# Kernel optimization log

Hardware: AMD Instinct MI355X
Metric: run time of the kernel (lower is better)

The kernel has to match this reference:

```python
import jax, jax.numpy as jnp
import numpy as np

D_MODEL = 256
K = 50                      # angle_k neighbors
TEMPERATURE = 10000.0
SCALE = 1.0
NUM_POS_FEATS = D_MODEL // 3 // 2 * 2   # 84
PADDING = D_MODEL - NUM_POS_FEATS * 3   # 4


def setup_inputs() -> dict:
    key = jax.random.key(0)
    ks = jax.random.split(key, 6)
    B, N, M = 4, 20000, 1024
    points = jax.random.normal(ks[0], (B, N, 3), jnp.float32)
    nodes = jax.random.normal(ks[1], (B, M, 3), jnp.float32)
    pn = jax.random.normal(ks[2], (B, N, 3), jnp.float32)
    nn_ = jax.random.normal(ks[3], (B, M, 3), jnp.float32)
    pn = pn / jnp.linalg.norm(pn, axis=-1, keepdims=True)
    nn_ = nn_ / jnp.linalg.norm(nn_, axis=-1, keepdims=True)
    W = jax.random.normal(ks[4], (4, D_MODEL), jnp.float32) * 0.5  # glo_proj weight (in,out)
    b = jax.random.normal(ks[5], (D_MODEL,), jnp.float32) * 0.1    # glo_proj bias
    return {"points": points, "nodes": nodes, "points_normals": pn,
            "nodes_normals": nn_, "W": W, "b": b}


def _signed_angle(v1, v2):
    sin_v = jnp.linalg.norm(jnp.cross(v1, v2), axis=-1)
    cos_v = jnp.sum(v1 * v2, axis=-1)
    ang = jnp.arctan2(sin_v, cos_v)
    return jnp.where(cos_v < 0, -ang, ang)


def _ppf_features(points, nodes, pn, nn_):
    # points (N,3), nodes (M,3); KNN gather then PPF angles -> (M,K,4)
    d2 = jnp.sum((nodes[:, None, :] - points[None, :, :]) ** 2, axis=-1)  # (M,N)
    _, knn_idx = jax.lax.top_k(-d2, K)          # (M,K) nearest points per node
    knn_pts = points[knn_idx]                   # (M,K,3) irregular gather
    knn_nrm = pn[knn_idx]                       # (M,K,3)
    ij = knn_pts - nodes[:, None, :]            # (M,K,3)
    d = jnp.linalg.norm(ij, axis=-1) * SCALE    # (M,K)
    n1 = jnp.broadcast_to(nn_[:, None, :], ij.shape)
    a_n1_d = _signed_angle(ij, n1)
    a_n2_d = _signed_angle(-ij, knn_nrm)
    a_n1_n2 = _signed_angle(n1, knn_nrm)
    return jnp.stack([d, a_n1_d, a_n2_d, a_n1_n2], axis=-1)  # (M,K,4)


def reference(points, nodes, points_normals, nodes_normals, W, b):
    # --- global embedding: PPF features -> Linear(4,D) -> max over K ---
    feats = jax.vmap(_ppf_features)(points, nodes, points_normals, nodes_normals)
    feats = jax.lax.stop_gradient(feats)        # original uses @torch.no_grad()
    glob = jnp.max(feats @ W + b, axis=-2)      # (B,M,D)
    # --- local embedding: sinusoidal position encoding of node coords ---
    dim_t = jnp.arange(NUM_POS_FEATS, dtype=jnp.float32)
    dim_t = TEMPERATURE ** (2.0 * jnp.floor(dim_t / 2.0) / NUM_POS_FEATS)
    pos = (nodes * SCALE)[..., None] / dim_t    # (B,M,3,F)
    pos_emb = jnp.stack([jnp.sin(pos[..., 0::2]), jnp.cos(pos[..., 1::2])], axis=-1)
    pos_emb = pos_emb.reshape(nodes.shape[0], nodes.shape[1], -1)  # (B,M,3*F)
    pos_emb = jnp.pad(pos_emb, [(0, 0), (0, 0), (0, PADDING)])     # (B,M,D)
    return glob, pos_emb
```

## Files before the change

kernel.cpp:

```cpp
#include <hip/hip_runtime.h>

#define N_PTS    20000
#define M_NODES  1024
#define BATCH    4
#define NNODE    (BATCH * M_NODES)
#define K_NN     50
#define D_MODEL  256
#define NPF      84
#define CAP      768
#define SELWIN   96
#define NSMP     2048
#define WLO      26
#define WHI      50
#define TN        32
#define KB_PPT    10
#define KB_CHUNK  2560
#define KB_NCHUNK 8
#define LOCAL_CAP 128
#define OVF_FLAG  (1 << 20)

__device__ __forceinline__ float signed_angle(float ax, float ay, float az,
                                              float bx, float by, float bz) {
    float cx = ay * bz - az * by;
    float cy = az * bx - ax * bz;
    float cz = ax * by - ay * bx;
    float s = sqrtf(cx * cx + cy * cy + cz * cz);
    float c = ax * bx + ay * by + az * bz;
    float a = atan2f(s, c);
    return (c < 0.0f) ? -a : a;
}

__global__ __launch_bounds__(256) void ka_thresh(
    const float* __restrict__ points, const float* __restrict__ nodes,
    float* __restrict__ tws, int* __restrict__ gcount, float* __restrict__ out)
{
    __shared__ float s3[NSMP * 3];
    const int tid  = threadIdx.x;
    const int w    = tid >> 6;
    const int lane = tid & 63;
    const int bm   = blockIdx.x * 4 + w;
    const int b    = bm >> 10;
    const float* pts = points + (size_t)b * N_PTS * 3;

    {
        const float4* src = (const float4*)pts;
        float4* dst = (float4*)s3;
        #pragma unroll
        for (int k = 0; k < 6; ++k)
            dst[tid + 256 * k] = src[tid + 256 * k];
    }
    __syncthreads();

    const float nx = nodes[(size_t)bm * 3 + 0];
    const float ny = nodes[(size_t)bm * 3 + 1];
    const float nz = nodes[(size_t)bm * 3 + 2];

    unsigned short keys[32];
    #pragma unroll
    for (int s = 0; s < 32; ++s) {
        int j = lane + 64 * s;
        float dx = s3[3 * j + 0] - nx;
        float dy = s3[3 * j + 1] - ny;
        float dz = s3[3 * j + 2] - nz;
        float d2 = dx * dx + dy * dy + dz * dz;
        keys[s] = (unsigned short)(__float_as_uint(d2) >> 16);
    }

    unsigned lo = 0, hi = 0x7F81u, v = 0;
    for (int it = 0; it < 16; ++it) {
        unsigned mid = lo + ((hi - lo) >> 1);
        int c = 0;
        #pragma unroll
        for (int s = 0; s < 32; ++s) c += (int)((unsigned)keys[s] < mid);
        for (int off = 32; off; off >>= 1) c += __shfl_down(c, off);
        c = __shfl(c, 0);
        if (c >= WLO && c <= WHI) { v = mid; break; }
        if (c < WLO) lo = mid; else hi = mid;
        if (hi - lo <= 1u) break;
    }
    if (v == 0) v = hi;
    if (lane == 0) { tws[bm] = __uint_as_float(v << 16); gcount[bm] = 0; }

    #pragma unroll
    for (int r = 0; r < 4; ++r) {
        int d = lane + 64 * r;
        float pv = 0.0f;
        if (d < 3 * NPF) {
            int c2 = d / NPF, rr = d - c2 * NPF, i = rr >> 1;
            float nc = (c2 == 0) ? nx : ((c2 == 1) ? ny : nz);
            const float L2_10000 = 13.287712379549449f;
            float tinv = exp2f(-L2_10000 * (float)i / 42.0f);
            float x = nc * tinv;
            pv = (rr & 1) ? cosf(x) : sinf(x);
        }
        out[(size_t)NNODE * D_MODEL + (size_t)bm * D_MODEL + d] = pv;
    }
}

__global__ __launch_bounds__(256) void kb_scan(
    const float* __restrict__ points, const float* __restrict__ nodes,
    const float* __restrict__ tws, int* __restrict__ gcount,
    unsigned short* __restrict__ cand)
{
    __shared__ float4 snd[TN];
    __shared__ unsigned short sbuf[TN][LOCAL_CAP];
    __shared__ int scnt[TN];
    __shared__ int sbase[TN];

    const int tile = blockIdx.x;
    const int ch   = blockIdx.y;
    const int ngb  = tile * TN;
    const int b    = ngb >> 10;
    const int tid  = threadIdx.x;
    const float* pts = points + (size_t)b * N_PTS * 3;

    if (tid < TN) {
        int ng = ngb + tid;
        snd[tid] = make_float4(nodes[(size_t)ng * 3 + 0], nodes[(size_t)ng * 3 + 1],
                               nodes[(size_t)ng * 3 + 2], tws[ng]);
        scnt[tid] = 0;
    }
    __syncthreads();

    const int base0 = ch * KB_CHUNK;
    float px[KB_PPT], py[KB_PPT], pz[KB_PPT];
    #pragma unroll
    for (int p = 0; p < KB_PPT; ++p) {
        int j = base0 + p * 256 + tid;
        bool ok = j < N_PTS;
        int jj = ok ? j : 0;
        float vx = pts[jj * 3 + 0], vy = pts[jj * 3 + 1], vz = pts[jj * 3 + 2];
        px[p] = ok ? vx : 1e18f;
        py[p] = ok ? vy : 1e18f;
        pz[p] = ok ? vz : 1e18f;
    }

    for (int n = 0; n < TN; ++n) {
        float4 nd = snd[n];
        unsigned m = 0;
        #pragma unroll
        for (int p = 0; p < KB_PPT; ++p) {
            float dx = px[p] - nd.x, dy = py[p] - nd.y, dz = pz[p] - nd.z;
            float d2 = dx * dx + dy * dy + dz * dz;
            m |= (d2 < nd.w) ? (1u << p) : 0u;
        }
        if (m) {
            do {
                int p = __ffs(m) - 1; m &= m - 1;
                int q = atomicAdd(&scnt[n], 1);
                if (q < LOCAL_CAP)
                    sbuf[n][q] = (unsigned short)(base0 + p * 256 + tid);
            } while (m);
        }
    }
    __syncthreads();

    if (tid < TN) {
        int c = scnt[tid];
        int flag = (c > LOCAL_CAP) ? OVF_FLAG : 0;
        sbase[tid] = atomicAdd(&gcount[ngb + tid], c + flag);
        scnt[tid] = (c < LOCAL_CAP) ? c : LOCAL_CAP;
    }
    __syncthreads();

    const int wv = tid >> 6, lane = tid & 63;
    #pragma unroll
    for (int nn = 0; nn < TN / 4; ++nn) {
        int n = wv * (TN / 4) + nn;
        int c = scnt[n], gb = sbase[n];
        for (int s = lane; s < c; s += 64) {
            int pos = gb + s;
            if (pos < CAP)
                cand[(size_t)(ngb + n) * CAP + pos] = sbuf[n][s];
        }
    }
}

__global__ __launch_bounds__(256) void kc_select(
    const float* __restrict__ points, const float* __restrict__ nodes,
    const float* __restrict__ pnrm, const float* __restrict__ nnrm,
    const float* __restrict__ W, const float* __restrict__ bias,
    const float* __restrict__ tws, const int* __restrict__ gcount,
    const unsigned short* __restrict__ cand, float* __restrict__ out)
{
    __shared__ unsigned long long skeys[4][CAP];
    __shared__ float4 f4v[4][K_NN];
    __shared__ unsigned short selidx[4][K_NN];

    const int tid  = threadIdx.x;
    const int wv   = tid >> 6;
    const int lane = tid & 63;
    const int bm   = blockIdx.x * 4 + wv;
    const int b    = bm >> 10;
    const float* pts = points + (size_t)b * N_PTS * 3;
    const float* pnr = pnrm   + (size_t)b * N_PTS * 3;
    const float nx  = nodes[(size_t)bm * 3 + 0];
    const float ny  = nodes[(size_t)bm * 3 + 1];
    const float nz  = nodes[(size_t)bm * 3 + 2];
    const float n1x = nnrm[(size_t)bm * 3 + 0];
    const float n1y = nnrm[(size_t)bm * 3 + 1];
    const float n1z = nnrm[(size_t)bm * 3 + 2];

    auto d2bits = [&](int i) -> unsigned int {
        float dx = pts[i * 3 + 0] - nx;
        float dy = pts[i * 3 + 1] - ny;
        float dz = pts[i * 3 + 2] - nz;
        return __float_as_uint(dx * dx + dy * dy + dz * dz);
    };

    if (lane < K_NN) selidx[wv][lane] = 0;

    const unsigned long long INVALID = ~0ull;
    int cnt = gcount[bm];
    int nsel = 0;

    if (cnt >= K_NN && cnt <= CAP) {
        const unsigned short* cp = cand + (size_t)bm * CAP;
        unsigned long long key[12];
        #pragma unroll
        for (int r = 0; r < 12; ++r) {
            int s = r * 64 + lane;
            key[r] = INVALID;
            if (s < cnt) {
                int i = (int)cp[s];
                key[r] = ((unsigned long long)d2bits(i) << 32) | (unsigned int)i;
            }
        }

        unsigned long long tcut = INVALID;
        bool conv = (cnt <= SELWIN);
        if (!conv) {
            unsigned lo = 0, hi = __float_as_uint(tws[bm]);
            for (int it = 0; it < 32 && !conv; ++it) {
                unsigned mid = lo + ((hi - lo) >> 1);
                unsigned long long tm = (unsigned long long)mid << 32;
                int c = 0;
                #pragma unroll
                for (int r = 0; r < 12; ++r)
                    c += (int)__popcll(__ballot(key[r] < tm));
                if (c >= K_NN && c <= SELWIN) { tcut = tm; conv = true; }
                else if (c < K_NN) lo = mid;
                else hi = mid;
                if (hi - lo <= 1u) break;
            }
        }

        int run = 0;
        #pragma unroll
        for (int r = 0; r < 12; ++r) {
            bool p = key[r] < tcut;
            unsigned long long mask = __ballot(p);
            if (p) {
                int q = run + (int)__popcll(mask & ((1ull << lane) - 1ull));
                skeys[wv][q] = key[r];
            }
            run += (int)__popcll(mask);
        }
        nsel = run;
    } else {
        unsigned tb = __float_as_uint(tws[bm]);
        unsigned lo = 0, hi = 0x7F000000u, good = 0;
        bool haveLo = false, haveHi = false;
        if (cnt < K_NN) { lo = tb; haveLo = true; }
        else            { hi = tb; haveHi = true; }
        unsigned cur = tb;
        for (int a = 0; a < 40 && !good; ++a) {
            if (haveLo && !haveHi) {
                cur = (cur < 0x7E800000u) ? cur + 0x00800000u : 0x7F000000u;
            } else if (haveHi && !haveLo) {
                cur = (cur >= 0x00800000u) ? cur - 0x00800000u : (cur >> 1);
            } else {
                cur = lo + ((hi - lo) >> 1);
                if (hi - lo <= 1u) { good = hi; break; }
            }
            float tf = __uint_as_float(cur);
            int c = 0;
            for (int i0 = lane; i0 < N_PTS; i0 += 64) {
                float dx = pts[i0 * 3 + 0] - nx;
                float dy = pts[i0 * 3 + 1] - ny;
                float dz = pts[i0 * 3 + 2] - nz;
                c += (int)(dx * dx + dy * dy + dz * dz < tf);
            }
            for (int off = 32; off; off >>= 1) c += __shfl_down(c, off);
            c = __shfl(c, 0);
            if (c >= K_NN && c <= CAP) good = cur;
            else if (c < K_NN) { lo = cur; haveLo = true; }
            else               { hi = cur; haveHi = true; }
        }
        if (!good) good = haveHi ? hi : 0x7F000000u;
        int run = 0;
        for (int base = 0; base < N_PTS; base += 64) {
            int i0 = base + lane;
            bool pred = false;
            unsigned kb2 = 0;
            if (i0 < N_PTS) { kb2 = d2bits(i0); pred = kb2 < good; }
            unsigned long long mask = __ballot(pred);
            if (pred) {
                int q = run + (int)__popcll(mask & ((1ull << lane) - 1ull));
                if (q < CAP)
                    skeys[wv][q] = ((unsigned long long)kb2 << 32) | (unsigned int)i0;
            }
            run += (int)__popcll(mask);
        }
        nsel = run < CAP ? run : CAP;
    }
    __syncthreads();

    for (int s = lane; s < nsel; s += 64) {
        unsigned long long mk = skeys[wv][s];
        int rank = 0;
        for (int j = 0; j < nsel; ++j) rank += (int)(skeys[wv][j] < mk);
        if (rank < K_NN) selidx[wv][rank] = (unsigned short)mk;
    }
    __syncthreads();

    if (lane < K_NN) {
        int i = (int)selidx[wv][lane];
        float pxx = pts[i * 3 + 0], pyy = pts[i * 3 + 1], pzz = pts[i * 3 + 2];
        float qx = pnr[i * 3 + 0], qy = pnr[i * 3 + 1], qz = pnr[i * 3 + 2];
        float ijx = pxx - nx, ijy = pyy - ny, ijz = pzz - nz;
        float d = sqrtf(ijx * ijx + ijy * ijy + ijz * ijz);
        f4v[wv][lane] = make_float4(d,
                                    signed_angle(ijx, ijy, ijz, n1x, n1y, n1z),
                                    signed_angle(-ijx, -ijy, -ijz, qx, qy, qz),
                                    signed_angle(n1x, n1y, n1z, qx, qy, qz));
    }
    __syncthreads();

    {
        float w0[4], w1[4], w2[4], w3[4], bb[4], mx[4];
        #pragma unroll
        for (int q = 0; q < 4; ++q) {
            int d = lane + 64 * q;
            w0[q] = W[d]; w1[q] = W[D_MODEL + d];
            w2[q] = W[2 * D_MODEL + d]; w3[q] = W[3 * D_MODEL + d];
            bb[q] = bias[d]; mx[q] = -INFINITY;
        }
        #pragma unroll 5
        for (int k = 0; k < K_NN; ++k) {
            float4 f = f4v[wv][k];
            #pragma unroll
            for (int q = 0; q < 4; ++q)
                mx[q] = fmaxf(mx[q], f.x * w0[q] + f.y * w1[q] + f.z * w2[q] + f.w * w3[q]);
        }
        #pragma unroll
        for (int q = 0; q < 4; ++q)
            out[(size_t)bm * D_MODEL + lane + 64 * q] = mx[q] + bb[q];
    }
}

extern "C" void kernel_launch(void* const* d_in, const int* in_sizes, int n_in,
                              void* d_out, int out_size, void* d_ws, size_t ws_size,
                              hipStream_t stream) {
    const float* points = (const float*)d_in[0];
    const float* nodes  = (const float*)d_in[1];
    const float* pn     = (const float*)d_in[2];
    const float* nn     = (const float*)d_in[3];
    const float* W      = (const float*)d_in[4];
    const float* bias   = (const float*)d_in[5];
    float* out = (float*)d_out;

    char* ws = (char*)d_ws;
    float* tws = (float*)ws;
    int* gcount = (int*)(ws + 16384);
    unsigned short* cand = (unsigned short*)(ws + 32768);

    ka_thresh<<<dim3(NNODE / 4), dim3(256), 0, stream>>>(points, nodes, tws, gcount, out);
    kb_scan<<<dim3(NNODE / TN, KB_NCHUNK), dim3(256), 0, stream>>>(points, nodes, tws, gcount, cand);
    kc_select<<<dim3(NNODE / 4), dim3(256), 0, stream>>>(points, nodes, pn, nn, W, bias,
                                                         tws, gcount, cand, out);
}
```

Baseline: 74.20 us.

## Restructure KNN candidate scan with expanded-distance FMAs and contiguous vector loads

The candidate scan kernel now gives each thread 8 contiguous points, loaded as six float4 reads, instead of strided scalar loads. Point distance tests use the expanded form |p|^2 - 2p·n < t - |n|^2, evaluated with FMAs. Nodes are processed four at a time, held in registers rather than read from shared memory. The threshold is relaxed slightly so rounding in the expanded form cannot drop true neighbours, at the cost of a few extra candidates. The chunk geometry changes to 10 chunks of 2048 points to match the new per-thread layout.

```diff
diff --git a/kernel.cpp b/kernel.cpp
--- a/kernel.cpp
+++ b/kernel.cpp
@@ -13,9 +13,9 @@
 #define WLO      26
 #define WHI      50
 #define TN        32
-#define KB_PPT    10
-#define KB_CHUNK  2560
-#define KB_NCHUNK 8
+#define KB_PPT    8
+#define KB_CHUNK  2048
+#define KB_NCHUNK 10
 #define LOCAL_CAP 128
 #define OVF_FLAG  (1 << 20)
 
@@ -102,7 +102,6 @@
     const float* __restrict__ tws, int* __restrict__ gcount,
     unsigned short* __restrict__ cand)
 {
-    __shared__ float4 snd[TN];
     __shared__ unsigned short sbuf[TN][LOCAL_CAP];
     __shared__ int scnt[TN];
     __shared__ int sbase[TN];
@@ -114,43 +113,62 @@
     const int tid  = threadIdx.x;
     const float* pts = points + (size_t)b * N_PTS * 3;
 
-    if (tid < TN) {
-        int ng = ngb + tid;
-        snd[tid] = make_float4(nodes[(size_t)ng * 3 + 0], nodes[(size_t)ng * 3 + 1],
-                               nodes[(size_t)ng * 3 + 2], tws[ng]);
-        scnt[tid] = 0;
-    }
-    __syncthreads();
-
-    const int base0 = ch * KB_CHUNK;
-    float px[KB_PPT], py[KB_PPT], pz[KB_PPT];
+    if (tid < TN) scnt[tid] = 0;
+    __syncthreads();
+
+    const int j0 = ch * KB_CHUNK + tid * KB_PPT;
+    float px[KB_PPT], py[KB_PPT], pz[KB_PPT], pp[KB_PPT];
+    if (j0 < N_PTS) {
+        const float4* s4 = (const float4*)(pts + (size_t)j0 * 3);
+        float4 v0 = s4[0], v1 = s4[1], v2 = s4[2], v3 = s4[3], v4 = s4[4], v5 = s4[5];
+        px[0]=v0.x; py[0]=v0.y; pz[0]=v0.z;
+        px[1]=v0.w; py[1]=v1.x; pz[1]=v1.y;
+        px[2]=v1.z; py[2]=v1.w; pz[2]=v2.x;
+        px[3]=v2.y; py[3]=v2.z; pz[3]=v2.w;
+        px[4]=v3.x; py[4]=v3.y; pz[4]=v3.z;
+        px[5]=v3.w; py[5]=v4.x; pz[5]=v4.y;
+        px[6]=v4.z; py[6]=v4.w; pz[6]=v5.x;
+        px[7]=v5.y; py[7]=v5.z; pz[7]=v5.w;
+    } else {
+        #pragma unroll
+        for (int p = 0; p < KB_PPT; ++p) { px[p]=1e18f; py[p]=1e18f; pz[p]=1e18f; }
+    }
     #pragma unroll
-    for (int p = 0; p < KB_PPT; ++p) {
-        int j = base0 + p * 256 + tid;
-        bool ok = j < N_PTS;
-        int jj = ok ? j : 0;
-        float vx = pts[jj * 3 + 0], vy = pts[jj * 3 + 1], vz = pts[jj * 3 + 2];
-        px[p] = ok ? vx : 1e18f;
-        py[p] = ok ? vy : 1e18f;
-        pz[p] = ok ? vz : 1e18f;
-    }
-
-    for (int n = 0; n < TN; ++n) {
-        float4 nd = snd[n];
-        unsigned m = 0;
+    for (int p = 0; p < KB_PPT; ++p)
+        pp[p] = px[p]*px[p] + py[p]*py[p] + pz[p]*pz[p];
+
+    for (int n0 = 0; n0 < TN; n0 += 4) {
+        float ax[4], ay[4], az[4], rhs[4];
+        #pragma unroll
+        for (int g = 0; g < 4; ++g) {
+            int ng = ngb + n0 + g;
+            float nx = nodes[ng * 3 + 0];
+            float ny = nodes[ng * 3 + 1];
+            float nz = nodes[ng * 3 + 2];
+            float t  = tws[ng];
+            ax[g] = -2.0f * nx; ay[g] = -2.0f * ny; az[g] = -2.0f * nz;
+            rhs[g] = t * 1.0001f + 3e-5f - (nx*nx + ny*ny + nz*nz);
+        }
+        unsigned msk[4] = {0u, 0u, 0u, 0u};
         #pragma unroll
         for (int p = 0; p < KB_PPT; ++p) {
-            float dx = px[p] - nd.x, dy = py[p] - nd.y, dz = pz[p] - nd.z;
-            float d2 = dx * dx + dy * dy + dz * dz;
-            m |= (d2 < nd.w) ? (1u << p) : 0u;
-        }
-        if (m) {
-            do {
-                int p = __ffs(m) - 1; m &= m - 1;
-                int q = atomicAdd(&scnt[n], 1);
-                if (q < LOCAL_CAP)
-                    sbuf[n][q] = (unsigned short)(base0 + p * 256 + tid);
-            } while (m);
+            #pragma unroll
+            for (int g = 0; g < 4; ++g) {
+                float s = fmaf(px[p], ax[g], fmaf(py[p], ay[g], fmaf(pz[p], az[g], pp[p])));
+                msk[g] |= (s < rhs[g]) ? (1u << p) : 0u;
+            }
+        }
+        #pragma unroll
+        for (int g = 0; g < 4; ++g) {
+            unsigned m = msk[g];
+            if (m) {
+                int n = n0 + g;
+                do {
+                    int p = __ffs(m) - 1; m &= m - 1;
+                    int q = atomicAdd(&scnt[n], 1);
+                    if (q < LOCAL_CAP) sbuf[n][q] = (unsigned short)(j0 + p);
+                } while (m);
+            }
         }
     }
     __syncthreads();
```

Result: slower. 79.18 us (+6.7%).
